# Optimization experiments

Hardware: AMD Instinct MI355X
Metric: run time of the kernel (lower is better)

## Reference

```python
import jax, jax.numpy as jnp
import numpy as np

DIL = (1, 2, 4, 8)  # dilations, num_dilation = 4
KS = 3              # kernel_size
EPS = 1e-5


def _unfold3(x, r):
    """nn.Unfold(3, dilation=r, padding=r): x [B,d,H,W] -> [B,d,9,H*W]."""
    B, d, H, W = x.shape
    xp = jnp.pad(x, ((0, 0), (0, 0), (r, r), (r, r)))
    cols = jnp.stack([xp[:, :, i * r:i * r + H, j * r:j * r + W]
                      for i in range(KS) for j in range(KS)], axis=2)
    return cols.reshape(B, d, KS * KS, H * W)


def setup_inputs() -> dict:
    key = jax.random.key(0)
    ks = jax.random.split(key, 8)
    B, C, H, W = 8, 256, 80, 80
    s = 0.05
    return {
        "x": jax.random.normal(ks[0], (B, C, H, W), jnp.float32),
        "qkv_w": jax.random.normal(ks[1], (3 * C, C), jnp.float32) * s,
        "qkv_b": jnp.zeros((3 * C,), jnp.float32),
        "fc_w": jax.random.normal(ks[2], (4, 4), jnp.float32) * 0.3,
        "fc_b": jnp.zeros((4,), jnp.float32),
        "ln_g": jnp.ones((C // 4,), jnp.float32),
        "ln_b": jnp.zeros((C // 4,), jnp.float32),
        "proj_w": jax.random.normal(ks[3], (C, C), jnp.float32) * s,
        "proj_b": jnp.zeros((C,), jnp.float32),
        "w1": jax.random.normal(ks[4], (2 * C, C), jnp.float32) * s,
        "bn1_g": jnp.ones((2 * C,), jnp.float32),
        "bn1_b": jnp.zeros((2 * C,), jnp.float32),
        "bn1_m": jnp.zeros((2 * C,), jnp.float32),
        "bn1_v": jnp.ones((2 * C,), jnp.float32),
        "w2": jax.random.normal(ks[5], (C, 2 * C), jnp.float32) * s,
        "bn2_g": jnp.ones((C,), jnp.float32),
        "bn2_b": jnp.zeros((C,), jnp.float32),
        "bn2_m": jnp.zeros((C,), jnp.float32),
        "bn2_v": jnp.ones((C,), jnp.float32),
    }


def _bn(z, g, b, m, v):
    # BatchNorm2d, eval mode (running stats), z is [B,C,H,W]
    inv = g / jnp.sqrt(v + EPS)
    return z * inv[None, :, None, None] + (b - m * inv)[None, :, None, None]


def _psablock(x, qkv_w, qkv_b, fc_w, fc_b, ln_g, ln_b, proj_w, proj_b,
              w1, bn1_g, bn1_b, bn1_m, bn1_v, w2, bn2_g, bn2_b, bn2_m, bn2_v):
    B, C, H, W = x.shape
    ND = len(DIL)
    Cd = C // ND                  # channels per dilation branch
    num_heads = 4
    hd = C // num_heads           # head_dim = 64
    nh = Cd // hd                 # heads per branch (= 1)
    scale = hd ** -0.5

    # qkv 1x1 conv: [B,3C,H,W] -> (3, ND, Cd) split
    qkv = jnp.einsum('bchw,oc->bohw', x, qkv_w) + qkv_b[None, :, None, None]
    qkv = qkv.reshape(B, 3, ND, Cd, H, W)

    feats = []
    for i, r in enumerate(DIL):
        q, k, v = qkv[:, 0, i], qkv[:, 1, i], qkv[:, 2, i]
        qh = q.reshape(B, nh, hd, H * W)                       # [B,nh,hd,N]
        kh = _unfold3(k, r).reshape(B, nh, hd, KS * KS, H * W)  # [B,nh,hd,9,N]
        vh = _unfold3(v, r).reshape(B, nh, hd, KS * KS, H * W)
        attn = jax.nn.softmax(
            jnp.einsum('bhcn,bhcjn->bhnj', qh, kh) * scale, axis=-1)
        out = jnp.einsum('bhnj,bhcjn->bnhc', attn, vh)          # [B,N,nh,hd]
        feats.append(out.reshape(B, H, W, Cd))

    # CrossScaleFusion: Linear over scale dim + residual + LayerNorm over Cd
    stacked = jnp.stack(feats, axis=3)                          # [B,H,W,S,Cd]
    fused = jnp.einsum('bhwsc,ts->bhwtc', stacked, fc_w) \
        + fc_b[None, None, None, :, None]
    fused = fused + stacked
    mu = fused.mean(-1, keepdims=True)
    var = fused.var(-1, keepdims=True)
    normed = (fused - mu) / jnp.sqrt(var + EPS) * ln_g + ln_b

    y2 = normed.reshape(B, H, W, C)
    y3 = jnp.einsum('bhwc,oc->bhwo', y2, proj_w) + proj_b
    attn_out = y3.transpose(0, 3, 1, 2)                         # [B,C,H,W]

    x1 = x + attn_out                                           # shortcut

    # FFN: Conv1x1(C->2C)+BN+SiLU, Conv1x1(2C->C)+BN, residual
    h = jnp.einsum('bchw,oc->bohw', x1, w1)
    h = jax.nn.silu(_bn(h, bn1_g, bn1_b, bn1_m, bn1_v))
    h = jnp.einsum('bchw,oc->bohw', h, w2)
    h = _bn(h, bn2_g, bn2_b, bn2_m, bn2_v)
    return x1 + h


def reference(x, qkv_w, qkv_b, fc_w, fc_b, ln_g, ln_b, proj_w, proj_b,
              w1, bn1_g, bn1_b, bn1_m, bn1_v, w2, bn2_g, bn2_b, bn2_m, bn2_v):
    return _psablock(x, qkv_w, qkv_b, fc_w, fc_b, ln_g, ln_b, proj_w, proj_b,
                     w1, bn1_g, bn1_b, bn1_m, bn1_v,
                     w2, bn2_g, bn2_b, bn2_m, bn2_v)
```

## Files before the change

### kernel.cpp

```cpp
#include <hip/hip_runtime.h>

#define EPS_F 1e-5f

typedef __attribute__((ext_vector_type(8))) short short8;
typedef __attribute__((ext_vector_type(4))) float f32x4;
typedef __attribute__((ext_vector_type(4))) unsigned short ushort4v;
typedef __attribute__((address_space(1))) void gvoid;
typedef __attribute__((address_space(3))) void svoid;

__device__ __forceinline__ float bf2f(unsigned short u){
    union { unsigned int i; float f; } v; v.i = ((unsigned int)u) << 16; return v.f;
}
__device__ __forceinline__ unsigned short f2bf(float f){
    union { float f; unsigned int i; } v; v.f = f;
    unsigned int r = v.i + 0x7FFFu + ((v.i >> 16) & 1u);
    return (unsigned short)(r >> 16);
}

template<int EPI>
__global__ __launch_bounds__(256, 2)
void mm_k(const short* __restrict__ A, const short* __restrict__ Bt,
          const int M, const int K,
          const float* __restrict__ p0, const float* __restrict__ p1,
          const float* __restrict__ p2, const float* __restrict__ p3,
          const float* __restrict__ resid,
          short* __restrict__ outT, float* __restrict__ outF)
{
    const int N = 6400;
    __shared__ short lsA[128 * 64];
    __shared__ short lsB[128 * 64];

    const int id = blockIdx.x;
    const int b  = id & 7;
    const int rr = id >> 3;
    const int n0 = (rr % 50) * 128;
    const int m0 = (rr / 50) * 128;
    const int t  = threadIdx.x;
    const int l  = t & 63;
    const int w  = t >> 6;
    const int wr = w >> 1, wc = w & 1;

    const short* Bb = Bt + (size_t)b * N * K;

    f32x4 acc[4][4];
    #pragma unroll
    for (int i = 0; i < 4; ++i)
        #pragma unroll
        for (int j = 0; j < 4; ++j) acc[i][j] = (f32x4){0.f, 0.f, 0.f, 0.f};

    const int rsub = l >> 3;
    const int csub = l & 7;

    for (int k0 = 0; k0 < K; k0 += 64) {
        #pragma unroll
        for (int q = 0; q < 4; ++q) {
            const int row = (w * 4 + q) * 8 + rsub;
            const int cs  = csub ^ (row & 7);
            const short* ga = A  + (size_t)(m0 + row) * K + k0 + (cs << 3);
            __builtin_amdgcn_global_load_lds((gvoid*)ga, (svoid*)(lsA + (w * 4 + q) * 512), 16, 0, 0);
            const short* gb = Bb + (size_t)(n0 + row) * K + k0 + (cs << 3);
            __builtin_amdgcn_global_load_lds((gvoid*)gb, (svoid*)(lsB + (w * 4 + q) * 512), 16, 0, 0);
        }
        __syncthreads();

        #pragma unroll
        for (int ks = 0; ks < 2; ++ks) {
            short8 av[4], bv[4];
            const int cfr = ks * 4 + (l >> 4);
            #pragma unroll
            for (int mi = 0; mi < 4; ++mi) {
                const int row = wr * 64 + mi * 16 + (l & 15);
                av[mi] = *(const short8*)&lsA[row * 64 + ((cfr ^ (row & 7)) << 3)];
            }
            #pragma unroll
            for (int ni = 0; ni < 4; ++ni) {
                const int row = wc * 64 + ni * 16 + (l & 15);
                bv[ni] = *(const short8*)&lsB[row * 64 + ((cfr ^ (row & 7)) << 3)];
            }
            #pragma unroll
            for (int mi = 0; mi < 4; ++mi)
                #pragma unroll
                for (int ni = 0; ni < 4; ++ni)
                    acc[mi][ni] = __builtin_amdgcn_mfma_f32_16x16x32_bf16(
                        av[mi], bv[ni], acc[mi][ni], 0, 0, 0);
        }
        __syncthreads();
    }

    const int mq = (l >> 4) * 4;
    const int nq = l & 15;
    #pragma unroll
    for (int mi = 0; mi < 4; ++mi) {
        const int mb = m0 + wr * 64 + mi * 16 + mq;
        float mul[4], add[4];
        #pragma unroll
        for (int j = 0; j < 4; ++j) {
            const int m = mb + j;
            if (EPI == 0 || EPI == 1) { mul[j] = 1.f; add[j] = p0[m]; }
            else { const float inv = p0[m] * rsqrtf(p3[m] + EPS_F);
                   mul[j] = inv; add[j] = p1[m] - p2[m] * inv; }
        }
        #pragma unroll
        for (int ni = 0; ni < 4; ++ni) {
            const int n = n0 + wc * 64 + ni * 16 + nq;
            float z[4];
            #pragma unroll
            for (int j = 0; j < 4; ++j) {
                z[j] = acc[mi][ni][j] * mul[j] + add[j];
                if (EPI == 2) z[j] = z[j] / (1.f + __expf(-z[j]));
                if (EPI == 1 || EPI == 3)
                    z[j] += resid[((size_t)b * M + mb + j) * N + n];
            }
            if (EPI == 0 || EPI == 1 || EPI == 2) {
                ushort4v u;
                #pragma unroll
                for (int j = 0; j < 4; ++j) u[j] = f2bf(z[j]);
                *(ushort4v*)&outT[((size_t)b * N + n) * M + mb] = u;
            }
            if (EPI == 1 || EPI == 3) {
                #pragma unroll
                for (int j = 0; j < 4; ++j)
                    outF[((size_t)b * M + mb + j) * N + n] = z[j];
            }
        }
    }
}

__global__ __launch_bounds__(256, 4)
void attn_k(const short* __restrict__ qkvt,
            const float* __restrict__ fc_w, const float* __restrict__ fc_b,
            const float* __restrict__ ln_g, const float* __restrict__ ln_b,
            short* __restrict__ y2t)
{
    __shared__ short st[4][64][64];

    const int id  = blockIdx.x;
    const int b   = id & 7;
    const int hw0 = (id >> 3) * 64;
    const int t   = threadIdx.x;
    const int di  = t >> 6;
    const int px  = t & 63;
    const int hw  = hw0 + px;
    const int yy  = hw / 80;
    const int xx  = hw % 80;
    const int r   = 1 << di;

    int   off[9];
    float okf[9];
    #pragma unroll
    for (int jy = 0; jy < 3; ++jy)
        #pragma unroll
        for (int jx = 0; jx < 3; ++jx) {
            const int ny = yy + (jy - 1) * r;
            const int nx = xx + (jx - 1) * r;
            const bool o = (ny >= 0) && (ny < 80) && (nx >= 0) && (nx < 80);
            okf[jy * 3 + jx] = o ? 1.f : 0.f;
            off[jy * 3 + jx] = o ? (ny * 80 + nx) : hw;
        }

    const short* qp = qkvt + ((size_t)(b * 6400 + hw)) * 768 + di * 64;

    float s[9];
    #pragma unroll
    for (int j = 0; j < 9; ++j) s[j] = 0.f;
    #pragma unroll
    for (int c8 = 0; c8 < 8; ++c8) {
        const short8 qv = *(const short8*)&qp[c8 * 8];
        float qf[8];
        #pragma unroll
        for (int u = 0; u < 8; ++u) qf[u] = bf2f((unsigned short)qv[u]);
        #pragma unroll
        for (int j = 0; j < 9; ++j) {
            const short8 kv = *(const short8*)(qkvt +
                ((size_t)(b * 6400 + off[j])) * 768 + 256 + di * 64 + c8 * 8);
            #pragma unroll
            for (int u = 0; u < 8; ++u)
                s[j] = fmaf(qf[u], bf2f((unsigned short)kv[u]), s[j]);
        }
    }
    #pragma unroll
    for (int j = 0; j < 9; ++j) s[j] *= okf[j] * 0.125f;

    float mx = s[0];
    #pragma unroll
    for (int j = 1; j < 9; ++j) mx = fmaxf(mx, s[j]);
    float e[9], sum = 0.f;
    #pragma unroll
    for (int j = 0; j < 9; ++j) { e[j] = __expf(s[j] - mx); sum += e[j]; }
    const float isum = 1.f / sum;
    float pe[9];
    #pragma unroll
    for (int j = 0; j < 9; ++j) pe[j] = e[j] * isum * okf[j];

    #pragma unroll
    for (int c8 = 0; c8 < 8; ++c8) {
        float o[8];
        #pragma unroll
        for (int u = 0; u < 8; ++u) o[u] = 0.f;
        #pragma unroll
        for (int j = 0; j < 9; ++j) {
            const short8 vv = *(const short8*)(qkvt +
                ((size_t)(b * 6400 + off[j])) * 768 + 512 + di * 64 + c8 * 8);
            #pragma unroll
            for (int u = 0; u < 8; ++u)
                o[u] = fmaf(pe[j], bf2f((unsigned short)vv[u]), o[u]);
        }
        short8 ov;
        #pragma unroll
        for (int u = 0; u < 8; ++u) ov[u] = (short)f2bf(o[u]);
        *(short8*)&st[di][px][(c8 ^ (px & 7)) << 3] = ov;
    }
    __syncthreads();

    float cw[4];
    #pragma unroll
    for (int s4 = 0; s4 < 4; ++s4) cw[s4] = fc_w[di * 4 + s4] + (s4 == di ? 1.f : 0.f);
    const float fb = fc_b[di];

    float mu = 0.f, sq = 0.f;
    #pragma unroll
    for (int c8 = 0; c8 < 8; ++c8) {
        const int cc = (c8 ^ (px & 7)) << 3;
        const short8 a0 = *(const short8*)&st[0][px][cc];
        const short8 a1 = *(const short8*)&st[1][px][cc];
        const short8 a2 = *(const short8*)&st[2][px][cc];
        const short8 a3 = *(const short8*)&st[3][px][cc];
        #pragma unroll
        for (int u = 0; u < 8; ++u) {
            float f = fb;
            f = fmaf(cw[0], bf2f((unsigned short)a0[u]), f);
            f = fmaf(cw[1], bf2f((unsigned short)a1[u]), f);
            f = fmaf(cw[2], bf2f((unsigned short)a2[u]), f);
            f = fmaf(cw[3], bf2f((unsigned short)a3[u]), f);
            mu += f; sq = fmaf(f, f, sq);
        }
    }
    mu *= (1.f / 64.f);
    const float var  = sq * (1.f / 64.f) - mu * mu;
    const float rstd = rsqrtf(var + EPS_F);

    short* yo = y2t + ((size_t)(b * 6400 + hw)) * 256 + di * 64;
    #pragma unroll
    for (int c8 = 0; c8 < 8; ++c8) {
        const int cc = (c8 ^ (px & 7)) << 3;
        const short8 a0 = *(const short8*)&st[0][px][cc];
        const short8 a1 = *(const short8*)&st[1][px][cc];
        const short8 a2 = *(const short8*)&st[2][px][cc];
        const short8 a3 = *(const short8*)&st[3][px][cc];
        short8 ov;
        #pragma unroll
        for (int u = 0; u < 8; ++u) {
            float f = fb;
            f = fmaf(cw[0], bf2f((unsigned short)a0[u]), f);
            f = fmaf(cw[1], bf2f((unsigned short)a1[u]), f);
            f = fmaf(cw[2], bf2f((unsigned short)a2[u]), f);
            f = fmaf(cw[3], bf2f((unsigned short)a3[u]), f);
            const int c = c8 * 8 + u;
            ov[u] = (short)f2bf((f - mu) * rstd * ln_g[c] + ln_b[c]);
        }
        *(short8*)&yo[c8 * 8] = ov;
    }
}

__global__ void xt_k(const float* __restrict__ x, short* __restrict__ xt)
{
    const int b  = blockIdx.y;
    const int hw = blockIdx.x * 256 + threadIdx.x;
    const float* xb = x + (size_t)b * 256 * 6400 + hw;
    short* o = xt + ((size_t)b * 6400 + hw) * 256;
    #pragma unroll 4
    for (int c8 = 0; c8 < 32; ++c8) {
        short8 v;
        #pragma unroll
        for (int u = 0; u < 8; ++u)
            v[u] = (short)f2bf(xb[(size_t)(c8 * 8 + u) * 6400]);
        *(short8*)&o[c8 * 8] = v;
    }
}

__global__ void wc_k(const float* __restrict__ a, const float* __restrict__ bb,
                     const float* __restrict__ c, const float* __restrict__ d,
                     short* __restrict__ o)
{
    const int i = blockIdx.x * 256 + threadIdx.x;
    float v;
    if      (i < 196608)  v = a[i];
    else if (i < 262144)  v = bb[i - 196608];
    else if (i < 393216)  v = c[i - 262144];
    else                  v = d[i - 393216];
    o[i] = (short)f2bf(v);
}

extern "C" void kernel_launch(void* const* d_in, const int* in_sizes, int n_in,
                              void* d_out, int out_size, void* d_ws, size_t ws_size,
                              hipStream_t stream)
{
    const float* x      = (const float*)d_in[0];
    const float* qkv_w  = (const float*)d_in[1];
    const float* qkv_b  = (const float*)d_in[2];
    const float* fc_w   = (const float*)d_in[3];
    const float* fc_b   = (const float*)d_in[4];
    const float* ln_g   = (const float*)d_in[5];
    const float* ln_b   = (const float*)d_in[6];
    const float* proj_w = (const float*)d_in[7];
    const float* proj_b = (const float*)d_in[8];
    const float* w1     = (const float*)d_in[9];
    const float* bn1_g  = (const float*)d_in[10];
    const float* bn1_b  = (const float*)d_in[11];
    const float* bn1_m  = (const float*)d_in[12];
    const float* bn1_v  = (const float*)d_in[13];
    const float* w2     = (const float*)d_in[14];
    const float* bn2_g  = (const float*)d_in[15];
    const float* bn2_b  = (const float*)d_in[16];
    const float* bn2_m  = (const float*)d_in[17];
    const float* bn2_v  = (const float*)d_in[18];
    float* out = (float*)d_out;

    const int B = 8;

    char* ws = (char*)d_ws;
    short* wqkvb  = (short*)(ws + 0);
    short* wprojb = wqkvb + 196608;
    short* w1b    = wprojb + 65536;
    short* w2b    = w1b + 131072;
    short* xt     = (short*)(ws + 1048576);
    short* qkvt   = (short*)(ws + 27262976);
    short* y2t    = (short*)(ws + 105906176);
    short* x1t    = (short*)(ws + 132120576);
    float* x1f    = (float*)(ws + 158334976);
    short* h      = qkvt;

    dim3 blk(256);

    wc_k<<<dim3(2048), blk, 0, stream>>>(qkv_w, proj_w, w1, w2, wqkvb);

    xt_k<<<dim3(25, B), blk, 0, stream>>>(x, xt);

    mm_k<0><<<dim3(50 * 6 * 8), blk, 0, stream>>>(
        wqkvb, xt, 768, 256, qkv_b, nullptr, nullptr, nullptr, nullptr,
        qkvt, nullptr);

    attn_k<<<dim3(800), blk, 0, stream>>>(qkvt, fc_w, fc_b, ln_g, ln_b, y2t);

    mm_k<1><<<dim3(50 * 2 * 8), blk, 0, stream>>>(
        wprojb, y2t, 256, 256, proj_b, nullptr, nullptr, nullptr, x,
        x1t, x1f);

    mm_k<2><<<dim3(50 * 4 * 8), blk, 0, stream>>>(
        w1b, x1t, 512, 256, bn1_g, bn1_b, bn1_m, bn1_v, nullptr,
        h, nullptr);

    mm_k<3><<<dim3(50 * 2 * 8), blk, 0, stream>>>(
        w2b, h, 256, 512, bn2_g, bn2_b, bn2_m, bn2_v, x1f,
        nullptr, out);
}
```

Baseline: 439.8 us.

## Split attention head channels across four lanes per pixel with shuffle reductions

The dilated-neighborhood attention kernel now assigns each pixel/dilation pair to four threads, each handling 16 of the 64 channels. Dot products and LayerNorm statistics are combined with cross-lane shuffles. Each block covers 16 pixels instead of 64, so the grid grows fourfold. This is meant to cut per-thread serial work and register pressure and to give better-coalesced wide loads, at the cost of extra shuffles and more blocks.

```diff
diff --git a/kernel.cpp b/kernel.cpp
--- a/kernel.cpp
+++ b/kernel.cpp
@@ -132,14 +132,15 @@
             const float* __restrict__ ln_g, const float* __restrict__ ln_b,
             short* __restrict__ y2t)
 {
-    __shared__ short st[4][64][64];
+    __shared__ short st[4][16][64];
 
     const int id  = blockIdx.x;
     const int b   = id & 7;
-    const int hw0 = (id >> 3) * 64;
+    const int hw0 = (id >> 3) * 16;
     const int t   = threadIdx.x;
+    const int px  = t & 15;
+    const int cg  = (t >> 4) & 3;
     const int di  = t >> 6;
-    const int px  = t & 63;
     const int hw  = hw0 + px;
     const int yy  = hw / 80;
     const int xx  = hw % 80;
@@ -158,28 +159,37 @@
             off[jy * 3 + jx] = o ? (ny * 80 + nx) : hw;
         }
 
-    const short* qp = qkvt + ((size_t)(b * 6400 + hw)) * 768 + di * 64;
+    const short* base = qkvt + (size_t)b * 6400 * 768;
+    const int ch = di * 64 + cg * 16;
+
+    const short8 qv0 = *(const short8*)(base + (size_t)hw * 768 + ch);
+    const short8 qv1 = *(const short8*)(base + (size_t)hw * 768 + ch + 8);
+    float qf[16];
+    #pragma unroll
+    for (int u = 0; u < 8; ++u) { qf[u] = bf2f((unsigned short)qv0[u]);
+                                  qf[8 + u] = bf2f((unsigned short)qv1[u]); }
 
     float s[9];
     #pragma unroll
-    for (int j = 0; j < 9; ++j) s[j] = 0.f;
-    #pragma unroll
-    for (int c8 = 0; c8 < 8; ++c8) {
-        const short8 qv = *(const short8*)&qp[c8 * 8];
-        float qf[8];
-        #pragma unroll
-        for (int u = 0; u < 8; ++u) qf[u] = bf2f((unsigned short)qv[u]);
-        #pragma unroll
-        for (int j = 0; j < 9; ++j) {
-            const short8 kv = *(const short8*)(qkvt +
-                ((size_t)(b * 6400 + off[j])) * 768 + 256 + di * 64 + c8 * 8);
-            #pragma unroll
-            for (int u = 0; u < 8; ++u)
-                s[j] = fmaf(qf[u], bf2f((unsigned short)kv[u]), s[j]);
-        }
-    }
-    #pragma unroll
-    for (int j = 0; j < 9; ++j) s[j] *= okf[j] * 0.125f;
+    for (int j = 0; j < 9; ++j) {
+        const short* kp = base + (size_t)off[j] * 768 + 256 + ch;
+        const short8 k0 = *(const short8*)kp;
+        const short8 k1 = *(const short8*)(kp + 8);
+        float a = 0.f;
+        #pragma unroll
+        for (int u = 0; u < 8; ++u) {
+            a = fmaf(qf[u],     bf2f((unsigned short)k0[u]), a);
+            a = fmaf(qf[8 + u], bf2f((unsigned short)k1[u]), a);
+        }
+        s[j] = a;
+    }
+
+    #pragma unroll
+    for (int j = 0; j < 9; ++j) {
+        s[j] += __shfl_xor(s[j], 16, 64);
+        s[j] += __shfl_xor(s[j], 32, 64);
+        s[j] *= okf[j] * 0.125f;
+    }
 
     float mx = s[0];
     #pragma unroll
@@ -192,24 +202,27 @@
     #pragma unroll
     for (int j = 0; j < 9; ++j) pe[j] = e[j] * isum * okf[j];
 
-    #pragma unroll
-    for (int c8 = 0; c8 < 8; ++c8) {
-        float o[8];
-        #pragma unroll
-        for (int u = 0; u < 8; ++u) o[u] = 0.f;
-        #pragma unroll
-        for (int j = 0; j < 9; ++j) {
-            const short8 vv = *(const short8*)(qkvt +
-                ((size_t)(b * 6400 + off[j])) * 768 + 512 + di * 64 + c8 * 8);
-            #pragma unroll
-            for (int u = 0; u < 8; ++u)
-                o[u] = fmaf(pe[j], bf2f((unsigned short)vv[u]), o[u]);
-        }
-        short8 ov;
-        #pragma unroll
-        for (int u = 0; u < 8; ++u) ov[u] = (short)f2bf(o[u]);
-        *(short8*)&st[di][px][(c8 ^ (px & 7)) << 3] = ov;
-    }
+    float o[16];
+    #pragma unroll
+    for (int u = 0; u < 16; ++u) o[u] = 0.f;
+    #pragma unroll
+    for (int j = 0; j < 9; ++j) {
+        const short* vp = base + (size_t)off[j] * 768 + 512 + ch;
+        const short8 v0 = *(const short8*)vp;
+        const short8 v1 = *(const short8*)(vp + 8);
+        #pragma unroll
+        for (int u = 0; u < 8; ++u) {
+            o[u]     = fmaf(pe[j], bf2f((unsigned short)v0[u]), o[u]);
+            o[8 + u] = fmaf(pe[j], bf2f((unsigned short)v1[u]), o[8 + u]);
+        }
+    }
+    short8 ov0, ov1;
+    #pragma unroll
+    for (int u = 0; u < 8; ++u) { ov0[u] = (short)f2bf(o[u]);
+                                  ov1[u] = (short)f2bf(o[8 + u]); }
+    short* sp = &st[di][px][0];
+    *(short8*)(sp + (((cg * 2)     ^ (px & 7)) << 3)) = ov0;
+    *(short8*)(sp + (((cg * 2 + 1) ^ (px & 7)) << 3)) = ov1;
     __syncthreads();
 
     float cw[4];
@@ -217,49 +230,40 @@
     for (int s4 = 0; s4 < 4; ++s4) cw[s4] = fc_w[di * 4 + s4] + (s4 == di ? 1.f : 0.f);
     const float fb = fc_b[di];
 
+    const int cc0 = ((cg * 2)     ^ (px & 7)) << 3;
+    const int cc1 = ((cg * 2 + 1) ^ (px & 7)) << 3;
+    float f[16];
+    #pragma unroll
+    for (int u = 0; u < 16; ++u) f[u] = fb;
+    #pragma unroll
+    for (int s4 = 0; s4 < 4; ++s4) {
+        const short8 a0 = *(const short8*)(&st[s4][px][0] + cc0);
+        const short8 a1 = *(const short8*)(&st[s4][px][0] + cc1);
+        #pragma unroll
+        for (int u = 0; u < 8; ++u) {
+            f[u]     = fmaf(cw[s4], bf2f((unsigned short)a0[u]), f[u]);
+            f[8 + u] = fmaf(cw[s4], bf2f((unsigned short)a1[u]), f[8 + u]);
+        }
+    }
     float mu = 0.f, sq = 0.f;
     #pragma unroll
-    for (int c8 = 0; c8 < 8; ++c8) {
-        const int cc = (c8 ^ (px & 7)) << 3;
-        const short8 a0 = *(const short8*)&st[0][px][cc];
-        const short8 a1 = *(const short8*)&st[1][px][cc];
-        const short8 a2 = *(const short8*)&st[2][px][cc];
-        const short8 a3 = *(const short8*)&st[3][px][cc];
-        #pragma unroll
-        for (int u = 0; u < 8; ++u) {
-            float f = fb;
-            f = fmaf(cw[0], bf2f((unsigned short)a0[u]), f);
-            f = fmaf(cw[1], bf2f((unsigned short)a1[u]), f);
-            f = fmaf(cw[2], bf2f((unsigned short)a2[u]), f);
-            f = fmaf(cw[3], bf2f((unsigned short)a3[u]), f);
-            mu += f; sq = fmaf(f, f, sq);
-        }
-    }
+    for (int u = 0; u < 16; ++u) { mu += f[u]; sq = fmaf(f[u], f[u], sq); }
+    mu += __shfl_xor(mu, 16, 64);  mu += __shfl_xor(mu, 32, 64);
+    sq += __shfl_xor(sq, 16, 64);  sq += __shfl_xor(sq, 32, 64);
     mu *= (1.f / 64.f);
     const float var  = sq * (1.f / 64.f) - mu * mu;
     const float rstd = rsqrtf(var + EPS_F);
 
-    short* yo = y2t + ((size_t)(b * 6400 + hw)) * 256 + di * 64;
-    #pragma unroll
-    for (int c8 = 0; c8 < 8; ++c8) {
-        const int cc = (c8 ^ (px & 7)) << 3;
-        const short8 a0 = *(const short8*)&st[0][px][cc];
-        const short8 a1 = *(const short8*)&st[1][px][cc];
-        const short8 a2 = *(const short8*)&st[2][px][cc];
-        const short8 a3 = *(const short8*)&st[3][px][cc];
-        short8 ov;
-        #pragma unroll
-        for (int u = 0; u < 8; ++u) {
-            float f = fb;
-            f = fmaf(cw[0], bf2f((unsigned short)a0[u]), f);
-            f = fmaf(cw[1], bf2f((unsigned short)a1[u]), f);
-            f = fmaf(cw[2], bf2f((unsigned short)a2[u]), f);
-            f = fmaf(cw[3], bf2f((unsigned short)a3[u]), f);
-            const int c = c8 * 8 + u;
-            ov[u] = (short)f2bf((f - mu) * rstd * ln_g[c] + ln_b[c]);
-        }
-        *(short8*)&yo[c8 * 8] = ov;
-    }
+    short* yo = y2t + ((size_t)(b * 6400 + hw)) * 256 + ch;
+    short8 y0, y1;
+    #pragma unroll
+    for (int u = 0; u < 8; ++u) {
+        const int c0 = cg * 16 + u, c1 = cg * 16 + 8 + u;
+        y0[u] = (short)f2bf((f[u]     - mu) * rstd * ln_g[c0] + ln_b[c0]);
+        y1[u] = (short)f2bf((f[8 + u] - mu) * rstd * ln_g[c1] + ln_b[c1]);
+    }
+    *(short8*)yo       = y0;
+    *(short8*)(yo + 8) = y1;
 }
 
 __global__ void xt_k(const float* __restrict__ x, short* __restrict__ xt)
@@ -340,7 +344,7 @@
         wqkvb, xt, 768, 256, qkv_b, nullptr, nullptr, nullptr, nullptr,
         qkvt, nullptr);
 
-    attn_k<<<dim3(800), blk, 0, stream>>>(qkvt, fc_w, fc_b, ln_g, ln_b, y2t);
+    attn_k<<<dim3(3200), blk, 0, stream>>>(qkvt, fc_w, fc_b, ln_g, ln_b, y2t);
 
     mm_k<1><<<dim3(50 * 2 * 8), blk, 0, stream>>>(
         wprojb, y2t, 256, 256, proj_b, nullptr, nullptr, nullptr, x,
```

New measurement: 381.7 us. -13.2%, faster.
